# Optimization experiments

Hardware: AMD Instinct MI355X
Metric: run time of the kernel (lower is better)

## Reference

```python
import jax, jax.numpy as jnp
import numpy as np

PAD_IDX = 1  # tgt_dict.stoi[PAD_WORD] in OpenNMT


def setup_inputs() -> dict:
    key = jax.random.key(0)
    ks = jax.random.split(key, 6)
    N, D = 2048, 1024          # batch_by_tlen (= tlen 64 * batch 32), rnn_size
    V = 50000                  # tgt vocab
    S, B, CV = 100, 32, 120    # src len, batch, dynamic copy vocab
    hidden = jax.random.normal(ks[0], (N, D), dtype=jnp.float32)
    # attention weights: softmax over src positions
    attn = jax.nn.softmax(jax.random.normal(ks[1], (N, S), dtype=jnp.float32), axis=-1)
    # src_map is one-hot: maps each src position of each batch to its dyn-vocab id
    src_ids = jax.random.randint(ks[2], (S, B), 0, CV)
    src_map = jax.nn.one_hot(src_ids, CV, dtype=jnp.float32)  # [S, B, CV]
    W = jax.random.normal(ks[3], (D, V), dtype=jnp.float32) / np.sqrt(D)
    b = jnp.zeros((V,), dtype=jnp.float32)
    w_copy = jax.random.normal(ks[4], (D, 1), dtype=jnp.float32) / np.sqrt(D)
    b_copy = jnp.zeros((1,), dtype=jnp.float32)
    return {"hidden": hidden, "attn": attn, "src_map": src_map,
            "W": W, "b": b, "w_copy": w_copy, "b_copy": b_copy}


def reference(hidden, attn, src_map, W, b, w_copy, b_copy):
    # hidden: [N, D], attn: [N, S], src_map: [S, B, CV], N = T*B (T-major)
    S, B, CV = src_map.shape
    logits = hidden @ W + b                              # [N, V]
    logits = logits.at[:, PAD_IDX].set(-jnp.inf)         # mask PAD
    prob = jax.nn.softmax(logits, axis=-1)               # [N, V]
    copy = jax.nn.sigmoid(hidden @ w_copy + b_copy)      # [N, 1]  p(copy)
    out_prob = prob * (1.0 - copy)                       # generate part
    mul_attn = (attn * copy).reshape(-1, B, S)           # [T, B, S]
    # bmm against (one-hot) src_map -> copy distribution over dyn vocab
    copy_prob = jnp.einsum('tbs,sbv->tbv', mul_attn, src_map).reshape(-1, CV)
    return jnp.concatenate([out_prob, copy_prob], axis=1)  # [N, V+CV]
```

## Files before the change

### kernel.cpp

```cpp
#include <hip/hip_runtime.h>
#include <hip/hip_bf16.h>
#include <math.h>

#define M_ 2048
#define K_ 1024
#define V_ 50000
#define VP_ 50048
#define CV_ 120
#define NC_ (V_ + CV_)
#define S_ 100
#define B_ 32
#define PAD_IDX_ 1

#define BM 256
#define BN 128
#define BK 64
#define NKT (K_ / BK)
#define NB_ (VP_ / BN)
#define NMT (M_ / BM)
#define NWG_ (NMT * NB_)
#define WPX_ (NWG_ / 8)
#define BUFB 24576
#define ELSB 136
#define PLSS 36
#define WEPI 17920
#define LN16 2.772588722239781f

#define WT_BLKS (782 * 16)
#define PREP_BLKS (M_ / 4)
#define IDS_BLKS (((S_ * B_) + 255) / 256)

typedef float f32x2 __attribute__((ext_vector_type(2)));
typedef float f32x4 __attribute__((ext_vector_type(4)));
typedef float f32x16 __attribute__((ext_vector_type(16)));
typedef int i32x4 __attribute__((ext_vector_type(4)));
typedef int i32x8 __attribute__((ext_vector_type(8)));
typedef unsigned int u32x2 __attribute__((ext_vector_type(2)));
typedef unsigned short ushort;
typedef unsigned char u8;

__device__ __forceinline__ void async_copy16(const void* g, void* l) {
    __builtin_amdgcn_global_load_lds(
        (const __attribute__((address_space(1))) void*)g,
        (__attribute__((address_space(3))) void*)l, 16, 0, 0);
}
#define SIG(row) (((row) >> 1) & 3)

__global__ __launch_bounds__(256)
void k_pre(const float* __restrict__ W, u8* __restrict__ Wt,
           const float* __restrict__ hidden, const float* __restrict__ w_copy,
           const float* __restrict__ b_copy, u8* __restrict__ Ab,
           float* __restrict__ cvec, const float* __restrict__ src_map,
           int* __restrict__ ids)
{
    int bx = blockIdx.x;
    int tid = threadIdx.x;
    if (bx < WT_BLKS) {
        __shared__ __align__(16) u8 t8[64][80];
        int v0 = (bx % 782) * 64;
        int k0 = (bx / 782) * 64;
        int kr = tid >> 4;
        int vq = tid & 15;
        int v4 = v0 + vq * 4;
#pragma unroll
        for (int i = 0; i < 4; ++i) {
            int k = k0 + kr + i * 16;
            f32x4 val = {};
            if (v4 < V_) val = *(const f32x4*)(W + (size_t)k * V_ + v4);
#pragma unroll
            for (int c = 0; c < 4; ++c) {
                int r = __builtin_amdgcn_cvt_pk_fp8_f32(val[c], 0.f, 0, 0);
                t8[vq * 4 + c][kr + i * 16] = (u8)r;
            }
        }
        __syncthreads();
        int vr = tid >> 2;
        int q  = tid & 3;
        i32x4 o = *(const i32x4*)(&t8[vr][q * 16]);
        *(i32x4*)(Wt + (size_t)(v0 + vr) * K_ + k0 + q * 16) = o;
    } else if (bx < WT_BLKS + PREP_BLKS) {
        int n = (bx - WT_BLKS) * 4 + (tid >> 6);
        int lane = tid & 63;
        const float* h = hidden + (size_t)n * K_;
        u8* arow = Ab + (size_t)n * K_;
        float s = 0.f;
#pragma unroll
        for (int g = 0; g < 2; ++g) {
            int gg = 2 * lane + g;
            f32x4 a = *(const f32x4*)(h + gg * 8);
            f32x4 b = *(const f32x4*)(h + gg * 8 + 4);
            f32x4 wa = *(const f32x4*)(w_copy + gg * 8);
            f32x4 wb = *(const f32x4*)(w_copy + gg * 8 + 4);
            s += a[0]*wa[0] + a[1]*wa[1] + a[2]*wa[2] + a[3]*wa[3]
               + b[0]*wb[0] + b[1]*wb[1] + b[2]*wb[2] + b[3]*wb[3];
            int p0 = __builtin_amdgcn_cvt_pk_fp8_f32(a[0], a[1], 0, 0);
            p0 = __builtin_amdgcn_cvt_pk_fp8_f32(a[2], a[3], p0, 1);
            int p1 = __builtin_amdgcn_cvt_pk_fp8_f32(b[0], b[1], 0, 0);
            p1 = __builtin_amdgcn_cvt_pk_fp8_f32(b[2], b[3], p1, 1);
            u32x2 pk; pk[0] = (unsigned)p0; pk[1] = (unsigned)p1;
            *(u32x2*)(arow + gg * 8) = pk;
        }
#pragma unroll
        for (int off = 32; off; off >>= 1) s += __shfl_down(s, off);
        if (lane == 0) cvec[n] = 1.f / (1.f + __expf(-(s + b_copy[0])));
    } else {
        int i = (bx - WT_BLKS - PREP_BLKS) * 256 + tid;
        if (i < S_ * B_) {
            const float* r = src_map + (size_t)i * CV_;
            int id = 0;
            for (int v = 0; v < CV_; ++v)
                if (r[v] > 0.5f) { id = v; break; }
            ids[i] = id;
        }
    }
}

template<bool E8P>
__global__ __launch_bounds__(256, 2)
void k_gemm_exp(const u8* __restrict__ A, const u8* __restrict__ Bt,
                const float* __restrict__ bias, float* __restrict__ out,
                u8* __restrict__ E8, float* __restrict__ part2)
{
    __shared__ __align__(16) u8 lds8[3 * BUFB];

    const int tid  = threadIdx.x;
    const int lane = tid & 63;
    const int wid  = tid >> 6;

    int orig = blockIdx.y * NMT + blockIdx.x;
    int nid  = (orig & 7) * WPX_ + (orig >> 3);
    const int m0 = (nid & 7) * BM;
    const int nb = nid >> 3;
    const int n0 = nb * BN;

    f32x16 acc[2][4] = {};

#define STAGE_A(d, kt)                                                        \
    do {                                                                      \
        _Pragma("unroll")                                                     \
        for (int j = 0; j < 4; ++j) {                                         \
            int g = j * 256 + tid; int row = g >> 2;                          \
            int ch = (g & 3) ^ SIG(row);                                      \
            async_copy16(A + (size_t)(m0 + row) * K_ + (kt) * BK + ch * 16,   \
                         &lds8[(d) * BUFB + (j * 256 + wid * 64) * 16]);      \
        }                                                                     \
    } while (0)
#define STAGE_B(d, kt)                                                        \
    do {                                                                      \
        _Pragma("unroll")                                                     \
        for (int j = 0; j < 2; ++j) {                                         \
            int g = j * 256 + tid; int row = g >> 2;                          \
            int ch = (g & 3) ^ SIG(row);                                      \
            async_copy16(Bt + (size_t)(n0 + row) * K_ + (kt) * BK + ch * 16,  \
                         &lds8[(d) * BUFB + 16384 + (j * 256 + wid * 64) * 16]); \
        }                                                                     \
    } while (0)

    STAGE_A(0, 0); STAGE_B(0, 0);
    STAGE_A(1, 1); STAGE_B(1, 1);

    const int rA  = lane & 31;
    const int kb  = lane >> 5;
    const int sig = (rA >> 1) & 3;

#pragma unroll
    for (int kt = 0; kt < NKT; ++kt) {
        const int cur = kt % 3;
        const int nxt = (kt + 2) % 3;
        __builtin_amdgcn_sched_barrier(0);
        if (kt < NKT - 1) asm volatile("s_waitcnt vmcnt(6)" ::: "memory");
        else              asm volatile("s_waitcnt vmcnt(0)" ::: "memory");
        __builtin_amdgcn_s_barrier();
        __builtin_amdgcn_sched_barrier(0);
        const u8* bufA = &lds8[cur * BUFB];
        const u8* bufB = bufA + 16384;
        i32x8 fa[2], fb[4];
#pragma unroll
        for (int mt = 0; mt < 2; ++mt) {
            int ro = (wid * 64 + mt * 32 + rA) * 64;
            i32x4 lo = *(const i32x4*)(bufA + ro + (((2 * kb + 0) ^ sig) << 4));
            i32x4 hi = *(const i32x4*)(bufA + ro + (((2 * kb + 1) ^ sig) << 4));
            fa[mt] = __builtin_shufflevector(lo, hi, 0, 1, 2, 3, 4, 5, 6, 7);
        }
        {
            int ro = rA * 64;
            i32x4 lo = *(const i32x4*)(bufB + ro + (((2 * kb + 0) ^ sig) << 4));
            i32x4 hi = *(const i32x4*)(bufB + ro + (((2 * kb + 1) ^ sig) << 4));
            fb[0] = __builtin_shufflevector(lo, hi, 0, 1, 2, 3, 4, 5, 6, 7);
        }
        if (kt < NKT - 2) STAGE_A(nxt, kt + 2);
        __builtin_amdgcn_s_setprio(1);
#pragma unroll
        for (int mt = 0; mt < 2; ++mt)
            acc[mt][0] = __builtin_amdgcn_mfma_scale_f32_32x32x64_f8f6f4(
                fa[mt], fb[0], acc[mt][0], 0, 0, 0, 127, 0, 127);
        __builtin_amdgcn_s_setprio(0);
        __builtin_amdgcn_sched_barrier(0);
#pragma unroll
        for (int nt = 1; nt < 4; ++nt) {
            int ro = (nt * 32 + rA) * 64;
            i32x4 lo = *(const i32x4*)(bufB + ro + (((2 * kb + 0) ^ sig) << 4));
            i32x4 hi = *(const i32x4*)(bufB + ro + (((2 * kb + 1) ^ sig) << 4));
            fb[nt] = __builtin_shufflevector(lo, hi, 0, 1, 2, 3, 4, 5, 6, 7);
        }
        if (kt < NKT - 2) STAGE_B(nxt, kt + 2);
        __builtin_amdgcn_s_setprio(1);
#pragma unroll
        for (int mt = 0; mt < 2; ++mt)
#pragma unroll
            for (int nt = 1; nt < 4; ++nt)
                acc[mt][nt] = __builtin_amdgcn_mfma_scale_f32_32x32x64_f8f6f4(
                    fa[mt], fb[nt], acc[mt][nt], 0, 0, 0, 127, 0, 127);
        __builtin_amdgcn_s_setprio(0);
    }
#undef STAGE_A
#undef STAGE_B

    __builtin_amdgcn_s_barrier();

    const int rbase = m0 + wid * 64;
    const int rhi   = (lane >> 5) * 4;
    float psum[2][16];
#pragma unroll
    for (int mt = 0; mt < 2; ++mt)
#pragma unroll
        for (int r = 0; r < 16; ++r) psum[mt][r] = 0.f;
    u8* Els8 = lds8 + wid * WEPI;
    float* Pls = (float*)(lds8 + wid * WEPI + 8704);
#pragma unroll
    for (int nt = 0; nt < 4; ++nt) {
        int gcol = n0 + nt * 32 + rA;
        bool live = (gcol < V_) && (gcol != PAD_IDX_);
        float bln = ((gcol < V_) ? bias[gcol] : 0.f) - LN16;
#pragma unroll
        for (int mt = 0; mt < 2; ++mt) {
#pragma unroll
            for (int r = 0; r < 16; ++r) {
                int crow = (r & 3) + 8 * (r >> 2) + rhi;
                float e = live ? __expf(acc[mt][nt][r] + bln) : 0.f;
                psum[mt][r] += e;
                if (E8P) {
                    Els8[(mt * 32 + crow) * ELSB + nt * 32 + rA] =
                        (u8)__builtin_amdgcn_cvt_pk_fp8_f32(e, 0.f, 0, 0);
                } else {
                    int grow = rbase + mt * 32 + crow;
                    if (gcol < V_) out[(size_t)grow * NC_ + gcol] = e;
                }
            }
        }
    }
    if (E8P) {
#pragma unroll
        for (int p = 0; p < 8; ++p) {
            int row_l = p * 8 + (lane >> 3);
            int g = lane & 7;
            i32x4 v = *(const i32x4*)(&Els8[row_l * ELSB + g * 16]);
            *(i32x4*)&E8[(size_t)(rbase + row_l) * VP_ + n0 + g * 16] = v;
        }
    }
#pragma unroll
    for (int mt = 0; mt < 2; ++mt)
#pragma unroll
        for (int r = 0; r < 16; ++r) {
            int crow = (r & 3) + 8 * (r >> 2) + rhi;
            Pls[(mt * 32 + crow) * PLSS + rA] = psum[mt][r];
        }
    const float* prow = Pls + lane * PLSS;
    f32x4 sv = {};
#pragma unroll
    for (int i = 0; i < 8; ++i) {
        f32x4 v = *(const f32x4*)(prow + i * 4);
        sv[0] += v[0]; sv[1] += v[1]; sv[2] += v[2]; sv[3] += v[3];
    }
    part2[(size_t)nb * M_ + rbase + lane] = sv[0] + sv[1] + sv[2] + sv[3];
}

template<bool E8P>
__global__ __launch_bounds__(256)
void k_finish(const u8* __restrict__ E8, const float* __restrict__ part2,
              const float* __restrict__ cvec, const float* __restrict__ attn,
              const int* __restrict__ ids, float* __restrict__ out)
{
    int n = blockIdx.y;
    int q = blockIdx.x;
    int tid = threadIdx.x;
    float c = cvec[n];
    float* row = out + (size_t)n * NC_;

    __shared__ float ws4[4];
    __shared__ float cp[CV_];
    if (q == 3 && tid < CV_) cp[tid] = 0.f;

    float s = 0.f;
    for (int p = tid; p < NB_; p += 256) s += part2[(size_t)p * M_ + n];
#pragma unroll
    for (int off = 32; off; off >>= 1) s += __shfl_down(s, off);
    if ((tid & 63) == 0) ws4[tid >> 6] = s;
    __syncthreads();
    float rowsum = ws4[0] + ws4[1] + ws4[2] + ws4[3];
    float sc = (1.f - c) / rowsum;

    if (q == 3 && tid < S_)
        atomicAdd(&cp[ids[tid * B_ + (n & (B_ - 1))]],
                  attn[(size_t)n * S_ + tid] * c);

    int i0 = q * 1563;
    int i1 = min(i0 + 1563, V_ / 8);
    if (E8P) {
        const u8* e8 = E8 + (size_t)n * VP_;
        for (int i = i0 + tid; i < i1; i += 256) {
            u32x2 w = *(const u32x2*)(e8 + i * 8);
            f32x2 a0 = __builtin_amdgcn_cvt_pk_f32_fp8(w[0], false);
            f32x2 a1 = __builtin_amdgcn_cvt_pk_f32_fp8(w[0], true);
            f32x2 a2 = __builtin_amdgcn_cvt_pk_f32_fp8(w[1], false);
            f32x2 a3 = __builtin_amdgcn_cvt_pk_f32_fp8(w[1], true);
            f32x4 o0, o1;
            o0[0] = a0[0] * sc; o0[1] = a0[1] * sc;
            o0[2] = a1[0] * sc; o0[3] = a1[1] * sc;
            o1[0] = a2[0] * sc; o1[1] = a2[1] * sc;
            o1[2] = a3[0] * sc; o1[3] = a3[1] * sc;
            __builtin_nontemporal_store(o0, (f32x4*)(row + i * 8));
            __builtin_nontemporal_store(o1, (f32x4*)(row + i * 8 + 4));
        }
    } else {
        for (int i = i0 * 2 + tid; i < i1 * 2; i += 256) {
            f32x4 v = *(const f32x4*)(row + i * 4);
            v[0]*=sc; v[1]*=sc; v[2]*=sc; v[3]*=sc;
            *(f32x4*)(row + i * 4) = v;
        }
    }
    if (q == 3) {
        __syncthreads();
        if (tid < CV_) row[V_ + tid] = cp[tid];
    }
}

extern "C" void kernel_launch(void* const* d_in, const int* in_sizes, int n_in,
                              void* d_out, int out_size, void* d_ws, size_t ws_size,
                              hipStream_t stream)
{
    const float* hidden  = (const float*)d_in[0];
    const float* attn    = (const float*)d_in[1];
    const float* src_map = (const float*)d_in[2];
    const float* W       = (const float*)d_in[3];
    const float* bias    = (const float*)d_in[4];
    const float* w_copy  = (const float*)d_in[5];
    const float* b_copy  = (const float*)d_in[6];
    float* out = (float*)d_out;

    size_t off = 0;
    u8* Wt = (u8*)((char*)d_ws + off); off += (size_t)VP_ * K_;
    u8* Ab = (u8*)((char*)d_ws + off); off += (size_t)M_ * K_;
    float* cvec = (float*)((char*)d_ws + off); off += M_ * 4;
    int*   ids  = (int*)((char*)d_ws + off);   off += 16384;
    float* part2 = (float*)((char*)d_ws + off); off += (size_t)NB_ * M_ * 4;
    u8* E8 = (u8*)((char*)d_ws + off);
    bool e8p = (off + (size_t)M_ * VP_) <= ws_size;

    k_pre<<<WT_BLKS + PREP_BLKS + IDS_BLKS, 256, 0, stream>>>(
        W, Wt, hidden, w_copy, b_copy, Ab, cvec, src_map, ids);

    dim3 gg(NMT, NB_);
    dim3 gf(4, M_);
    if (e8p) {
        k_gemm_exp<true><<<gg, 256, 0, stream>>>(Ab, Wt, bias, out, E8, part2);
        k_finish<true><<<gf, 256, 0, stream>>>(E8, part2, cvec, attn, ids, out);
    } else {
        k_gemm_exp<false><<<gg, 256, 0, stream>>>(Ab, Wt, bias, out, E8, part2);
        k_finish<false><<<gf, 256, 0, stream>>>((const u8*)out, part2, cvec, attn, ids, out);
    }
}
```

Measured before the change: 340.4 us.

## Split GEMM tile across 8 waves in a 4x2 grid instead of 4 waves

The 256x128 FP8 GEMM tile is now computed by 512 threads (8 waves arranged 4 along M by 2 along N), each wave owning a 64x64 subtile instead of 64x128. Staging loads, LDS epilogue slabs and the vmcnt wait are resized to match, and per-row partial sums are written per N-half, so the finish kernel reduces twice as many partials. This is meant to add latency hiding and parallelism per workgroup with fewer accumulators per wave. In exchange, each wave loads A fragments that its N-neighbour also loads, and the part2 buffer and its reduction double in size.

```diff
diff --git a/kernel.cpp b/kernel.cpp
--- a/kernel.cpp
+++ b/kernel.cpp
@@ -21,9 +21,9 @@
 #define NWG_ (NMT * NB_)
 #define WPX_ (NWG_ / 8)
 #define BUFB 24576
-#define ELSB 136
-#define PLSS 36
-#define WEPI 17920
+#define ELSB 80
+#define PLSS 34
+#define PSLAB 8704
 #define LN16 2.772588722239781f
 
 #define WT_BLKS (782 * 16)
@@ -116,7 +116,7 @@
 }
 
 template<bool E8P>
-__global__ __launch_bounds__(256, 2)
+__global__ __launch_bounds__(512, 4)
 void k_gemm_exp(const u8* __restrict__ A, const u8* __restrict__ Bt,
                 const float* __restrict__ bias, float* __restrict__ out,
                 u8* __restrict__ E8, float* __restrict__ part2)
@@ -126,6 +126,8 @@
     const int tid  = threadIdx.x;
     const int lane = tid & 63;
     const int wid  = tid >> 6;
+    const int wm   = wid >> 1;
+    const int wn   = wid & 1;
 
     int orig = blockIdx.y * NMT + blockIdx.x;
     int nid  = (orig & 7) * WPX_ + (orig >> 3);
@@ -133,27 +135,24 @@
     const int nb = nid >> 3;
     const int n0 = nb * BN;
 
-    f32x16 acc[2][4] = {};
+    f32x16 acc[2][2] = {};
 
 #define STAGE_A(d, kt)                                                        \
     do {                                                                      \
         _Pragma("unroll")                                                     \
-        for (int j = 0; j < 4; ++j) {                                         \
-            int g = j * 256 + tid; int row = g >> 2;                          \
+        for (int j = 0; j < 2; ++j) {                                         \
+            int g = j * 512 + tid; int row = g >> 2;                          \
             int ch = (g & 3) ^ SIG(row);                                      \
             async_copy16(A + (size_t)(m0 + row) * K_ + (kt) * BK + ch * 16,   \
-                         &lds8[(d) * BUFB + (j * 256 + wid * 64) * 16]);      \
+                         &lds8[(d) * BUFB + g * 16]);                         \
         }                                                                     \
     } while (0)
 #define STAGE_B(d, kt)                                                        \
     do {                                                                      \
-        _Pragma("unroll")                                                     \
-        for (int j = 0; j < 2; ++j) {                                         \
-            int g = j * 256 + tid; int row = g >> 2;                          \
-            int ch = (g & 3) ^ SIG(row);                                      \
-            async_copy16(Bt + (size_t)(n0 + row) * K_ + (kt) * BK + ch * 16,  \
-                         &lds8[(d) * BUFB + 16384 + (j * 256 + wid * 64) * 16]); \
-        }                                                                     \
+        int g = tid; int row = g >> 2;                                        \
+        int ch = (g & 3) ^ SIG(row);                                          \
+        async_copy16(Bt + (size_t)(n0 + row) * K_ + (kt) * BK + ch * 16,      \
+                     &lds8[(d) * BUFB + 16384 + g * 16]);                     \
     } while (0)
 
     STAGE_A(0, 0); STAGE_B(0, 0);
@@ -168,22 +167,22 @@
         const int cur = kt % 3;
         const int nxt = (kt + 2) % 3;
         __builtin_amdgcn_sched_barrier(0);
-        if (kt < NKT - 1) asm volatile("s_waitcnt vmcnt(6)" ::: "memory");
+        if (kt < NKT - 1) asm volatile("s_waitcnt vmcnt(3)" ::: "memory");
         else              asm volatile("s_waitcnt vmcnt(0)" ::: "memory");
         __builtin_amdgcn_s_barrier();
         __builtin_amdgcn_sched_barrier(0);
         const u8* bufA = &lds8[cur * BUFB];
         const u8* bufB = bufA + 16384;
-        i32x8 fa[2], fb[4];
+        i32x8 fa[2], fb[2];
 #pragma unroll
         for (int mt = 0; mt < 2; ++mt) {
-            int ro = (wid * 64 + mt * 32 + rA) * 64;
+            int ro = (wm * 64 + mt * 32 + rA) * 64;
             i32x4 lo = *(const i32x4*)(bufA + ro + (((2 * kb + 0) ^ sig) << 4));
             i32x4 hi = *(const i32x4*)(bufA + ro + (((2 * kb + 1) ^ sig) << 4));
             fa[mt] = __builtin_shufflevector(lo, hi, 0, 1, 2, 3, 4, 5, 6, 7);
         }
         {
-            int ro = rA * 64;
+            int ro = (wn * 64 + rA) * 64;
             i32x4 lo = *(const i32x4*)(bufB + ro + (((2 * kb + 0) ^ sig) << 4));
             i32x4 hi = *(const i32x4*)(bufB + ro + (((2 * kb + 1) ^ sig) << 4));
             fb[0] = __builtin_shufflevector(lo, hi, 0, 1, 2, 3, 4, 5, 6, 7);
@@ -196,21 +195,18 @@
                 fa[mt], fb[0], acc[mt][0], 0, 0, 0, 127, 0, 127);
         __builtin_amdgcn_s_setprio(0);
         __builtin_amdgcn_sched_barrier(0);
-#pragma unroll
-        for (int nt = 1; nt < 4; ++nt) {
-            int ro = (nt * 32 + rA) * 64;
+        {
+            int ro = (wn * 64 + 32 + rA) * 64;
             i32x4 lo = *(const i32x4*)(bufB + ro + (((2 * kb + 0) ^ sig) << 4));
             i32x4 hi = *(const i32x4*)(bufB + ro + (((2 * kb + 1) ^ sig) << 4));
-            fb[nt] = __builtin_shufflevector(lo, hi, 0, 1, 2, 3, 4, 5, 6, 7);
+            fb[1] = __builtin_shufflevector(lo, hi, 0, 1, 2, 3, 4, 5, 6, 7);
         }
         if (kt < NKT - 2) STAGE_B(nxt, kt + 2);
         __builtin_amdgcn_s_setprio(1);
 #pragma unroll
         for (int mt = 0; mt < 2; ++mt)
-#pragma unroll
-            for (int nt = 1; nt < 4; ++nt)
-                acc[mt][nt] = __builtin_amdgcn_mfma_scale_f32_32x32x64_f8f6f4(
-                    fa[mt], fb[nt], acc[mt][nt], 0, 0, 0, 127, 0, 127);
+            acc[mt][1] = __builtin_amdgcn_mfma_scale_f32_32x32x64_f8f6f4(
+                fa[mt], fb[1], acc[mt][1], 0, 0, 0, 127, 0, 127);
         __builtin_amdgcn_s_setprio(0);
     }
 #undef STAGE_A
@@ -218,18 +214,19 @@
 
     __builtin_amdgcn_s_barrier();
 
-    const int rbase = m0 + wid * 64;
+    const int rbase = m0 + wm * 64;
+    const int cbase = n0 + wn * 64;
     const int rhi   = (lane >> 5) * 4;
     float psum[2][16];
 #pragma unroll
     for (int mt = 0; mt < 2; ++mt)
 #pragma unroll
         for (int r = 0; r < 16; ++r) psum[mt][r] = 0.f;
-    u8* Els8 = lds8 + wid * WEPI;
-    float* Pls = (float*)(lds8 + wid * WEPI + 8704);
-#pragma unroll
-    for (int nt = 0; nt < 4; ++nt) {
-        int gcol = n0 + nt * 32 + rA;
+    u8* Els8 = lds8 + wid * PSLAB;
+    float* Pls = (float*)(lds8 + wid * PSLAB);
+#pragma unroll
+    for (int nt = 0; nt < 2; ++nt) {
+        int gcol = cbase + nt * 32 + rA;
         bool live = (gcol < V_) && (gcol != PAD_IDX_);
         float bln = ((gcol < V_) ? bias[gcol] : 0.f) - LN16;
 #pragma unroll
@@ -251,13 +248,14 @@
     }
     if (E8P) {
 #pragma unroll
-        for (int p = 0; p < 8; ++p) {
-            int row_l = p * 8 + (lane >> 3);
-            int g = lane & 7;
+        for (int p = 0; p < 4; ++p) {
+            int row_l = p * 16 + (lane >> 2);
+            int g = lane & 3;
             i32x4 v = *(const i32x4*)(&Els8[row_l * ELSB + g * 16]);
-            *(i32x4*)&E8[(size_t)(rbase + row_l) * VP_ + n0 + g * 16] = v;
-        }
-    }
+            *(i32x4*)&E8[(size_t)(rbase + row_l) * VP_ + cbase + g * 16] = v;
+        }
+    }
+    __builtin_amdgcn_sched_barrier(0);
 #pragma unroll
     for (int mt = 0; mt < 2; ++mt)
 #pragma unroll
@@ -272,7 +270,7 @@
         f32x4 v = *(const f32x4*)(prow + i * 4);
         sv[0] += v[0]; sv[1] += v[1]; sv[2] += v[2]; sv[3] += v[3];
     }
-    part2[(size_t)nb * M_ + rbase + lane] = sv[0] + sv[1] + sv[2] + sv[3];
+    part2[((size_t)nb * 2 + wn) * M_ + rbase + lane] = sv[0] + sv[1] + sv[2] + sv[3];
 }
 
 template<bool E8P>
@@ -292,7 +290,7 @@
     if (q == 3 && tid < CV_) cp[tid] = 0.f;
 
     float s = 0.f;
-    for (int p = tid; p < NB_; p += 256) s += part2[(size_t)p * M_ + n];
+    for (int p = tid; p < 2 * NB_; p += 256) s += part2[(size_t)p * M_ + n];
 #pragma unroll
     for (int off = 32; off; off >>= 1) s += __shfl_down(s, off);
     if ((tid & 63) == 0) ws4[tid >> 6] = s;
@@ -353,7 +351,7 @@
     u8* Ab = (u8*)((char*)d_ws + off); off += (size_t)M_ * K_;
     float* cvec = (float*)((char*)d_ws + off); off += M_ * 4;
     int*   ids  = (int*)((char*)d_ws + off);   off += 16384;
-    float* part2 = (float*)((char*)d_ws + off); off += (size_t)NB_ * M_ * 4;
+    float* part2 = (float*)((char*)d_ws + off); off += (size_t)NB_ * 2 * M_ * 4;
     u8* E8 = (u8*)((char*)d_ws + off);
     bool e8p = (off + (size_t)M_ * VP_) <= ws_size;
 
@@ -363,10 +361,10 @@
     dim3 gg(NMT, NB_);
     dim3 gf(4, M_);
     if (e8p) {
-        k_gemm_exp<true><<<gg, 256, 0, stream>>>(Ab, Wt, bias, out, E8, part2);
+        k_gemm_exp<true><<<gg, 512, 0, stream>>>(Ab, Wt, bias, out, E8, part2);
         k_finish<true><<<gf, 256, 0, stream>>>(E8, part2, cvec, attn, ids, out);
     } else {
-        k_gemm_exp<false><<<gg, 256, 0, stream>>>(Ab, Wt, bias, out, E8, part2);
+        k_gemm_exp<false><<<gg, 512, 0, stream>>>(Ab, Wt, bias, out, E8, part2);
         k_finish<false><<<gf, 256, 0, stream>>>((const u8*)out, part2, cvec, attn, ids, out);
     }
 }
```

After: 334.1 us. Within noise of the previous version (-1.8%).

## Double-buffer LDS fragments in registers and prefetch next k-tile during MFMAs

Applied to the files above, without the earlier changes.

Restructures the GEMM main loop so the fragments for the next k-tile are loaded from LDS into a second register set while the MFMAs run on the current set. The split LDS reads and two-phase MFMA issue are replaced by one fragment-read block and a single 2x4 MFMA group per iteration, and both A and B global prefetches are issued together. The aim is to hide LDS read latency behind matrix math. In exchange, each iteration now waits for all outstanding global loads (vmcnt(0)), which shortens the effective global prefetch distance. It also raises register pressure from the doubled fragment storage.

```diff
diff --git a/kernel.cpp b/kernel.cpp
--- a/kernel.cpp
+++ b/kernel.cpp
@@ -156,65 +156,61 @@
         }                                                                     \
     } while (0)
 
-    STAGE_A(0, 0); STAGE_B(0, 0);
-    STAGE_A(1, 1); STAGE_B(1, 1);
-
     const int rA  = lane & 31;
     const int kb  = lane >> 5;
     const int sig = (rA >> 1) & 3;
 
+    i32x8 fa[2][2], fb[2][4];
+#define RDFRAGS(b, s)                                                         \
+    do {                                                                      \
+        const u8* bufA_ = &lds8[(b) * BUFB];                                  \
+        const u8* bufB_ = bufA_ + 16384;                                      \
+        _Pragma("unroll")                                                     \
+        for (int mt = 0; mt < 2; ++mt) {                                      \
+            int ro = (wid * 64 + mt * 32 + rA) * 64;                          \
+            i32x4 lo = *(const i32x4*)(bufA_ + ro + (((2*kb+0)^sig) << 4));   \
+            i32x4 hi = *(const i32x4*)(bufA_ + ro + (((2*kb+1)^sig) << 4));   \
+            fa[s][mt] = __builtin_shufflevector(lo, hi, 0,1,2,3,4,5,6,7);     \
+        }                                                                     \
+        _Pragma("unroll")                                                     \
+        for (int nt = 0; nt < 4; ++nt) {                                      \
+            int ro = (nt * 32 + rA) * 64;                                     \
+            i32x4 lo = *(const i32x4*)(bufB_ + ro + (((2*kb+0)^sig) << 4));   \
+            i32x4 hi = *(const i32x4*)(bufB_ + ro + (((2*kb+1)^sig) << 4));   \
+            fb[s][nt] = __builtin_shufflevector(lo, hi, 0,1,2,3,4,5,6,7);     \
+        }                                                                     \
+    } while (0)
+
+    STAGE_A(0, 0); STAGE_B(0, 0);
+    STAGE_A(1, 1); STAGE_B(1, 1);
+    asm volatile("s_waitcnt vmcnt(6)" ::: "memory");
+    __builtin_amdgcn_s_barrier();
+    RDFRAGS(0, 0);
+
 #pragma unroll
     for (int kt = 0; kt < NKT; ++kt) {
-        const int cur = kt % 3;
-        const int nxt = (kt + 2) % 3;
+        const int cs = kt & 1, ns = cs ^ 1;
         __builtin_amdgcn_sched_barrier(0);
-        if (kt < NKT - 1) asm volatile("s_waitcnt vmcnt(6)" ::: "memory");
-        else              asm volatile("s_waitcnt vmcnt(0)" ::: "memory");
+        asm volatile("s_waitcnt vmcnt(0)" ::: "memory");
         __builtin_amdgcn_s_barrier();
         __builtin_amdgcn_sched_barrier(0);
-        const u8* bufA = &lds8[cur * BUFB];
-        const u8* bufB = bufA + 16384;
-        i32x8 fa[2], fb[4];
-#pragma unroll
-        for (int mt = 0; mt < 2; ++mt) {
-            int ro = (wid * 64 + mt * 32 + rA) * 64;
-            i32x4 lo = *(const i32x4*)(bufA + ro + (((2 * kb + 0) ^ sig) << 4));
-            i32x4 hi = *(const i32x4*)(bufA + ro + (((2 * kb + 1) ^ sig) << 4));
-            fa[mt] = __builtin_shufflevector(lo, hi, 0, 1, 2, 3, 4, 5, 6, 7);
-        }
-        {
-            int ro = rA * 64;
-            i32x4 lo = *(const i32x4*)(bufB + ro + (((2 * kb + 0) ^ sig) << 4));
-            i32x4 hi = *(const i32x4*)(bufB + ro + (((2 * kb + 1) ^ sig) << 4));
-            fb[0] = __builtin_shufflevector(lo, hi, 0, 1, 2, 3, 4, 5, 6, 7);
-        }
-        if (kt < NKT - 2) STAGE_A(nxt, kt + 2);
+        if (kt < NKT - 2) {
+            const int nxt = (kt + 2) % 3;
+            STAGE_A(nxt, kt + 2); STAGE_B(nxt, kt + 2);
+        }
+        if (kt < NKT - 1) RDFRAGS((kt + 1) % 3, ns);
         __builtin_amdgcn_s_setprio(1);
 #pragma unroll
         for (int mt = 0; mt < 2; ++mt)
-            acc[mt][0] = __builtin_amdgcn_mfma_scale_f32_32x32x64_f8f6f4(
-                fa[mt], fb[0], acc[mt][0], 0, 0, 0, 127, 0, 127);
-        __builtin_amdgcn_s_setprio(0);
-        __builtin_amdgcn_sched_barrier(0);
-#pragma unroll
-        for (int nt = 1; nt < 4; ++nt) {
-            int ro = (nt * 32 + rA) * 64;
-            i32x4 lo = *(const i32x4*)(bufB + ro + (((2 * kb + 0) ^ sig) << 4));
-            i32x4 hi = *(const i32x4*)(bufB + ro + (((2 * kb + 1) ^ sig) << 4));
-            fb[nt] = __builtin_shufflevector(lo, hi, 0, 1, 2, 3, 4, 5, 6, 7);
-        }
-        if (kt < NKT - 2) STAGE_B(nxt, kt + 2);
-        __builtin_amdgcn_s_setprio(1);
-#pragma unroll
-        for (int mt = 0; mt < 2; ++mt)
-#pragma unroll
-            for (int nt = 1; nt < 4; ++nt)
+#pragma unroll
+            for (int nt = 0; nt < 4; ++nt)
                 acc[mt][nt] = __builtin_amdgcn_mfma_scale_f32_32x32x64_f8f6f4(
-                    fa[mt], fb[nt], acc[mt][nt], 0, 0, 0, 127, 0, 127);
+                    fa[cs][mt], fb[cs][nt], acc[mt][nt], 0, 0, 0, 127, 0, 127);
         __builtin_amdgcn_s_setprio(0);
     }
 #undef STAGE_A
 #undef STAGE_B
+#undef RDFRAGS
 
     __builtin_amdgcn_s_barrier();
 
```

New measurement: 510.9 us. 1.5x slower.
